# Optimization experiments

Hardware: AMD Instinct MI355X
Metric: run time of the kernel (lower is better)

Reference implementation:

```python
import jax, jax.numpy as jnp
import numpy as np

B, N, F_IN, H, FO = 4, 2048, 256, 4, 64


def setup_inputs() -> dict:
    key = jax.random.key(0)
    k1, k2, k3, k4, k5 = jax.random.split(key, 5)
    x = jax.random.normal(k1, (B, N, F_IN), dtype=jnp.float32)
    # random 0/1 adjacency with self-loops so every row of softmax is finite
    adj = jax.random.randint(k2, (N, N), 0, 2).astype(jnp.float32)
    adj = jnp.maximum(adj, jnp.eye(N, dtype=jnp.float32))
    # parameters (xavier-uniform style)
    lim_w = float(np.sqrt(6.0 / (F_IN + H * FO)))
    W = jax.random.uniform(k3, (F_IN, H * FO), minval=-lim_w, maxval=lim_w, dtype=jnp.float32)
    lim_a = float(np.sqrt(6.0 / (H + FO)))
    a_src = jax.random.uniform(k4, (H, FO), minval=-lim_a, maxval=lim_a, dtype=jnp.float32)
    a_dst = jax.random.uniform(k5, (H, FO), minval=-lim_a, maxval=lim_a, dtype=jnp.float32)
    return {"x": x, "adj": adj, "W": W, "a_src": a_src, "a_dst": a_dst}


def reference(x, adj, W, a_src, a_dst):
    # h: (B, N, H, FO)
    h = (x @ W).reshape(B, N, H, FO)
    attn_src = jnp.einsum("bnhf,hf->bnh", h, a_src)  # (B,N,H)
    attn_dst = jnp.einsum("bnhf,hf->bnh", h, a_dst)  # (B,N,H)
    # scores[b,i,j,h] = src[b,i,h] + dst[b,j,h]
    scores = attn_src[:, :, None, :] + attn_dst[:, None, :, :]
    scores = jax.nn.leaky_relu(scores, negative_slope=0.2)
    mask = (adj == 0)[None, :, :, None]  # (1,N,N,1)
    scores = jnp.where(mask, -jnp.inf, scores)
    attn = jax.nn.softmax(scores, axis=2)  # softmax over neighbors j
    # dropout is identity in eval mode / p=0
    out = jnp.einsum("bijh,bjhf->bihf", attn, h)  # (B,N,H,FO)
    return out.reshape(B, N, H * FO)  # concat=True
```

## Files before the change

### kernel.cpp

```cpp
#include <hip/hip_runtime.h>
#include <hip/hip_bf16.h>
#include <math.h>

#define B 4
#define N 2048
#define FIN 256
#define H 4
#define FO 64
#define M (B*N)
#define HF (H*FO)

typedef __attribute__((ext_vector_type(8))) short short8;
typedef __attribute__((ext_vector_type(8))) _Float16 half8;
typedef __attribute__((ext_vector_type(2))) _Float16 half2v;
typedef __attribute__((ext_vector_type(4))) float float4v;
typedef __attribute__((ext_vector_type(4))) int int4v;

#if __has_builtin(__builtin_amdgcn_exp2f)
#define EXP2(x) __builtin_amdgcn_exp2f(x)
#else
#define EXP2(x) exp2f(x)
#endif

static __device__ __forceinline__ void split_pair(float x0, float x1,
                                                  unsigned int& hi, unsigned int& lo) {
  unsigned int u0 = __builtin_bit_cast(unsigned int, x0);
  unsigned int u1 = __builtin_bit_cast(unsigned int, x1);
  hi = (u0 >> 16) | (u1 & 0xffff0000u);
  float h0 = __builtin_bit_cast(float, u0 & 0xffff0000u);
  float h1 = __builtin_bit_cast(float, u1 & 0xffff0000u);
  unsigned int l0 = __builtin_bit_cast(unsigned int, x0 - h0);
  unsigned int l1 = __builtin_bit_cast(unsigned int, x1 - h1);
  lo = (l0 >> 16) | (l1 & 0xffff0000u);
}

static __device__ __forceinline__ unsigned int fenc(float f) {
  unsigned int b = __builtin_bit_cast(unsigned int, f);
  return (b & 0x80000000u) ? ~b : (b | 0x80000000u);
}
static __device__ __forceinline__ float fdec(unsigned int e) {
  unsigned int b = (e & 0x80000000u) ? (e & 0x7fffffffu) : ~e;
  return __builtin_bit_cast(float, b);
}

static __device__ __forceinline__ unsigned int bit_sext(unsigned int v, int k) {
#if __has_builtin(__builtin_amdgcn_sbfe)
  return (unsigned int)__builtin_amdgcn_sbfe((int)v, k, 1);
#else
  return (unsigned int)(((int)(v << (31 - k))) >> 31);
#endif
}
static __device__ __forceinline__ unsigned int pm2(unsigned int mk, int p) {
  return __builtin_amdgcn_perm(bit_sext(mk, 2 * p + 1), bit_sext(mk, 2 * p), 0x07060302u);
}
static __device__ __forceinline__ unsigned int f16pk(float a, float b) {
  auto h = __builtin_amdgcn_cvt_pkrtz(a, b);
  return __builtin_bit_cast(unsigned int, h);
}

__global__ __launch_bounds__(256) void prep_wx(const float* __restrict__ Wsrc,
                                               const float* __restrict__ X,
                                               unsigned short* __restrict__ Wf_hi,
                                               unsigned short* __restrict__ Wf_lo,
                                               unsigned short* __restrict__ Xf_hi,
                                               unsigned short* __restrict__ Xf_lo,
                                               unsigned int* __restrict__ DmaxEnc) {
  const int blk = blockIdx.x;
  const int t = threadIdx.x;
  __shared__ float lds[64][65];
  if (blk < 16) {
    if (blk == 0 && t < 16) DmaxEnc[t] = 0u;
    const int k0 = (blk >> 2) * 64;
    const int h  = blk & 3;
    const int n0 = h * 64;
    const int c4 = (t & 15) * 4;
    #pragma unroll
    for (int rep = 0; rep < 4; ++rep) {
      const int kl = (t >> 4) + 16 * rep;
      const float4 v = *(const float4*)(Wsrc + (size_t)(k0 + kl) * HF + n0 + c4);
      lds[kl][c4 + 0] = v.x; lds[kl][c4 + 1] = v.y;
      lds[kl][c4 + 2] = v.z; lds[kl][c4 + 3] = v.w;
    }
    __syncthreads();
    #pragma unroll
    for (int rep = 0; rep < 2; ++rep) {
      const int s   = t + rep * 256;
      const int kcl = s >> 8;
      const int tt  = (s >> 6) & 3;
      const int ln  = s & 63;
      const int fL  = tt * 16 + (ln & 15);
      const int kb  = kcl * 32 + (ln >> 4) * 8;
      unsigned int hv[4], lv[4];
      #pragma unroll
      for (int p = 0; p < 4; ++p)
        split_pair(lds[kb + 2 * p][fL], lds[kb + 2 * p + 1][fL], hv[p], lv[p]);
      const size_t off = ((((size_t)h * 8 + (k0 >> 5) + kcl) * 4 + tt) << 9) + ln * 8;
      *(uint4*)(Wf_hi + off) = make_uint4(hv[0], hv[1], hv[2], hv[3]);
      *(uint4*)(Wf_lo + off) = make_uint4(lv[0], lv[1], lv[2], lv[3]);
    }
    return;
  }
  const int xb2   = blk - 16;
  const int xblk  = xb2 >> 2;
  const int ktile = xb2 & 3;
  const int mrow0 = xblk * 64;
  const int k0 = ktile * 64;
  const int c4 = (t & 15) * 4;
  #pragma unroll
  for (int rep = 0; rep < 4; ++rep) {
    const int rl = (t >> 4) + 16 * rep;
    const float4 v = *(const float4*)(X + (size_t)(mrow0 + rl) * FIN + k0 + c4);
    lds[rl][c4 + 0] = v.x; lds[rl][c4 + 1] = v.y;
    lds[rl][c4 + 2] = v.z; lds[rl][c4 + 3] = v.w;
  }
  __syncthreads();
  #pragma unroll
  for (int rep = 0; rep < 2; ++rep) {
    const int s   = t + rep * 256;
    const int mt  = s >> 7;
    const int kcl = (s >> 6) & 1;
    const int ln  = s & 63;
    const int mrl = mt * 16 + (ln & 15);
    const int kb  = kcl * 32 + (ln >> 4) * 8;
    unsigned int hv[4], lv[4];
    #pragma unroll
    for (int p = 0; p < 4; ++p)
      split_pair(lds[mrl][kb + 2 * p], lds[mrl][kb + 2 * p + 1], hv[p], lv[p]);
    const size_t off = (((size_t)(xblk * 4 + mt) * 8 + (ktile * 2 + kcl)) << 9) + ln * 8;
    *(uint4*)(Xf_hi + off) = make_uint4(hv[0], hv[1], hv[2], hv[3]);
    *(uint4*)(Xf_lo + off) = make_uint4(lv[0], lv[1], lv[2], lv[3]);
  }
}

__global__ __launch_bounds__(256) void gemm_fused(const unsigned short* __restrict__ Xf_hi,
                                                  const unsigned short* __restrict__ Xf_lo,
                                                  const unsigned short* __restrict__ Wf_hi,
                                                  const unsigned short* __restrict__ Wf_lo,
                                                  const float* __restrict__ adj,
                                                  const float* __restrict__ a_src,
                                                  const float* __restrict__ a_dst,
                                                  float* __restrict__ Srcv,
                                                  unsigned short* __restrict__ E1h,
                                                  unsigned short* __restrict__ E2h,
                                                  unsigned int* __restrict__ DmaxEnc,
                                                  unsigned long long* __restrict__ packed,
                                                  unsigned short* __restrict__ Hf) {
  if (blockIdx.x >= 512) {
    const int row = blockIdx.x - 512;
    const int pw = threadIdx.x >> 6, pl = threadIdx.x & 63;
    const float* ar = adj + (size_t)row * N;
    for (int c = pw; c < N / 64; c += 4) {
      unsigned long long m = __ballot(ar[c * 64 + pl] != 0.f);
      if (pl == 0) packed[(size_t)row * (N / 64) + c] = m;
    }
    return;
  }
  __shared__ unsigned short sh[64][72];
  __shared__ float smax[4];
  const int xcd  = blockIdx.x & 7;
  const int slot = blockIdx.x >> 3;
  const int mb = xcd * 16 + (slot >> 2);
  const int h  = slot & 3;
  const int w = threadIdx.x >> 6, lane = threadIdx.x & 63;
  const int fl = lane & 15, quad = lane >> 4;
  const float L2E = 1.4426950408889634f;

  const float4v zero = {0.f, 0.f, 0.f, 0.f};
  float4v acc[4] = {zero, zero, zero, zero};

  const size_t abase = (((size_t)(mb * 4 + w) * 8) << 9) + lane * 8;
  #pragma unroll
  for (int kc = 0; kc < 8; ++kc) {
    const short8 Ahi = *(const short8*)(Xf_hi + abase + ((size_t)kc << 9));
    const short8 Alo = *(const short8*)(Xf_lo + abase + ((size_t)kc << 9));
    #pragma unroll
    for (int t = 0; t < 4; ++t) {
      const size_t woff = ((((size_t)h * 8 + kc) * 4 + t) << 9) + lane * 8;
      const short8 Bhi = *(const short8*)(Wf_hi + woff);
      const short8 Blo = *(const short8*)(Wf_lo + woff);
      acc[t] = __builtin_amdgcn_mfma_f32_16x16x32_bf16(Ahi, Bhi, acc[t], 0, 0, 0);
      acc[t] = __builtin_amdgcn_mfma_f32_16x16x32_bf16(Alo, Bhi, acc[t], 0, 0, 0);
      acc[t] = __builtin_amdgcn_mfma_f32_16x16x32_bf16(Ahi, Blo, acc[t], 0, 0, 0);
    }
  }

  const int bb  = (mb * 64) >> 11;
  const int n0w = (mb * 64) & (N - 1);
  const int bh  = bb * H + h;
  float as[4], ad[4];
  #pragma unroll
  for (int t = 0; t < 4; ++t) {
    as[t] = a_src[h * FO + t * 16 + fl];
    ad[t] = a_dst[h * FO + t * 16 + fl];
  }
  float wmax = -INFINITY;
  #pragma unroll
  for (int reg = 0; reg < 4; ++reg) {
    float sv = 0.f, dv = 0.f;
    #pragma unroll
    for (int t = 0; t < 4; ++t) {
      sv = fmaf(acc[t][reg], as[t], sv);
      dv = fmaf(acc[t][reg], ad[t], dv);
    }
    #pragma unroll
    for (int off = 1; off <= 8; off <<= 1) {
      sv += __shfl_xor(sv, off, 64);
      dv += __shfl_xor(dv, off, 64);
    }
    wmax = fmaxf(wmax, dv);
    if (fl == 0) {
      const int node = n0w + w * 16 + quad * 4 + reg;
      Srcv[(bh << 11) + node] = sv;
      const unsigned int eu = f16pk(EXP2(dv * L2E),
                                    EXP2(dv * (0.2f * L2E)));
      E1h[(bh << 11) + node] = (unsigned short)(eu & 0xffffu);
      E2h[(bh << 11) + node] = (unsigned short)(eu >> 16);
    }
  }
  wmax = fmaxf(wmax, __shfl_xor(wmax, 16, 64));
  wmax = fmaxf(wmax, __shfl_xor(wmax, 32, 64));
  if (lane == 0) smax[w] = wmax;

  #pragma unroll
  for (int t = 0; t < 4; ++t) {
    const int nl = w * 16 + quad * 4;
    *(unsigned int*)&sh[t * 16 + fl][nl]     = f16pk(acc[t][0], acc[t][1]);
    *(unsigned int*)&sh[t * 16 + fl][nl + 2] = f16pk(acc[t][2], acc[t][3]);
  }
  __syncthreads();
  if (threadIdx.x == 0) {
    const float bmax = fmaxf(fmaxf(smax[0], smax[1]), fmaxf(smax[2], smax[3]));
    atomicMax(DmaxEnc + bh, fenc(bmax));
  }
  const int jc0 = n0w >> 5;
  #pragma unroll
  for (int rep = 0; rep < 2; ++rep) {
    const int s = (int)threadIdx.x + rep * 256;
    const int jcl = s >> 8;
    const int tt  = (s >> 6) & 3;
    const int ln  = s & 63;
    const int f    = tt * 16 + (ln & 15);
    const int node = jcl * 32 + (ln >> 4) * 8;
    unsigned short* dsth = Hf + (((size_t)bh * 64 + jc0 + jcl) * 4 + tt) * 512 + ln * 8;
    *(uint4*)dsth = *(const uint4*)&sh[f][node];
  }
}

__global__ __launch_bounds__(512) void gat_mfma(const unsigned char* __restrict__ pb,
                                                const float* __restrict__ Src,
                                                const unsigned short* __restrict__ E1h,
                                                const unsigned short* __restrict__ E2h,
                                                const unsigned int* __restrict__ DmaxEnc,
                                                const unsigned short* __restrict__ Hf,
                                                float* __restrict__ out) {
  const int xcd  = blockIdx.x & 7;
  const int slot = blockIdx.x >> 3;
  const int b    = xcd >> 1;
  const int i0   = ((xcd & 1) * 32 + slot) * 32;
  const int w    = threadIdx.x >> 6;
  const int lane = threadIdx.x & 63;
  const int h    = w & 3;
  const int jh   = w >> 2;
  const int bh   = b * H + h;
  const int fl   = lane & 15;
  const int kk   = (lane >> 4) * 8;
  const float L2E = 1.4426950408889634f;

  const int row0 = i0 + fl;
  const int row1 = i0 + 16 + fl;
  const float dmx = fdec(DmaxEnc[bh]);
  const float s0 = Src[(bh << 11) + row0];
  const float s1 = Src[(bh << 11) + row1];
  const float u0 = s0 + dmx, m0 = fmaxf(u0, 0.2f * u0);
  const float u1 = s1 + dmx, m1 = fmaxf(u1, 0.2f * u1);
  const float c1a = EXP2((s0 - m0) * L2E), c2a = EXP2((0.2f * s0 - m0) * L2E);
  const float c1b = EXP2((s1 - m1) * L2E), c2b = EXP2((0.2f * s1 - m1) * L2E);
  const half2v c1a2 = {(_Float16)c1a, (_Float16)c1a};
  const half2v c2a2 = {(_Float16)c2a, (_Float16)c2a};
  const half2v c1b2 = {(_Float16)c1b, (_Float16)c1b};
  const half2v c2b2 = {(_Float16)c2b, (_Float16)c2b};
  const unsigned char* pb0 = pb + (size_t)row0 * (N / 8);
  const unsigned char* pb1 = pb + (size_t)row1 * (N / 8);
  const unsigned short* hfb = Hf + (size_t)bh * 64 * 2048 + lane * 8;
  const unsigned short* e1b = E1h + (bh << 11);
  const unsigned short* e2b = E2h + (bh << 11);

  half8 ones;
  #pragma unroll
  for (int jj = 0; jj < 8; ++jj) ones[jj] = (_Float16)1.0f;

  const float4v zero = {0.f, 0.f, 0.f, 0.f};
  float4v acc[2][4];
  float4v accL[2];
  #pragma unroll
  for (int rt = 0; rt < 2; ++rt) {
    accL[rt] = zero;
    #pragma unroll
    for (int t = 0; t < 4; ++t) acc[rt][t] = zero;
  }

  const int jbeg = jh * (N / 2);
  short8 nb0, nb1, nb2, nb3;
  uint4 nE1, nE2;
  unsigned int nm0, nm1;
  {
    const unsigned short* hc = hfb + (size_t)(jbeg >> 5) * 2048;
    nb0 = *(const short8*)(hc + 0 * 512);
    nb1 = *(const short8*)(hc + 1 * 512);
    nb2 = *(const short8*)(hc + 2 * 512);
    nb3 = *(const short8*)(hc + 3 * 512);
    nE1 = *(const uint4*)(e1b + jbeg + kk);
    nE2 = *(const uint4*)(e2b + jbeg + kk);
    nm0 = pb0[(jbeg + kk) >> 3];
    nm1 = pb1[(jbeg + kk) >> 3];
  }

  for (int it = 0; it < 32; ++it) {
    const short8 b0 = nb0, b1 = nb1, b2 = nb2, b3 = nb3;
    const uint4 E1q = nE1, E2q = nE2;
    const unsigned int mk0 = nm0, mk1 = nm1;
    if (it < 31) {
      const int jn = jbeg + (it + 1) * 32;
      const unsigned short* hc = hfb + (size_t)(jn >> 5) * 2048;
      nb0 = *(const short8*)(hc + 0 * 512);
      nb1 = *(const short8*)(hc + 1 * 512);
      nb2 = *(const short8*)(hc + 2 * 512);
      nb3 = *(const short8*)(hc + 3 * 512);
      nE1 = *(const uint4*)(e1b + jn + kk);
      nE2 = *(const uint4*)(e2b + jn + kk);
      nm0 = pb0[(jn + kk) >> 3];
      nm1 = pb1[(jn + kk) >> 3];
    }
    const unsigned int e1w[4] = {E1q.x, E1q.y, E1q.z, E1q.w};
    const unsigned int e2w[4] = {E2q.x, E2q.y, E2q.z, E2q.w};
    int p0i[4], p1i[4];
    #pragma unroll
    for (int p = 0; p < 4; ++p) {
      const half2v e1 = __builtin_bit_cast(half2v, e1w[p]);
      const half2v e2 = __builtin_bit_cast(half2v, e2w[p]);
      const half2v wa = __builtin_elementwise_max(c1a2 * e1, c2a2 * e2);
      const half2v wb = __builtin_elementwise_max(c1b2 * e1, c2b2 * e2);
      p0i[p] = (int)(__builtin_bit_cast(unsigned int, wa) & pm2(mk0, p));
      p1i[p] = (int)(__builtin_bit_cast(unsigned int, wb) & pm2(mk1, p));
    }
    const half8 p0 = __builtin_bit_cast(half8, (int4v){p0i[0], p0i[1], p0i[2], p0i[3]});
    const half8 p1 = __builtin_bit_cast(half8, (int4v){p1i[0], p1i[1], p1i[2], p1i[3]});
    const half8 hb0 = __builtin_bit_cast(half8, b0);
    const half8 hb1 = __builtin_bit_cast(half8, b1);
    const half8 hb2 = __builtin_bit_cast(half8, b2);
    const half8 hb3 = __builtin_bit_cast(half8, b3);
    acc[0][0] = __builtin_amdgcn_mfma_f32_16x16x32_f16(p0, hb0, acc[0][0], 0, 0, 0);
    acc[0][1] = __builtin_amdgcn_mfma_f32_16x16x32_f16(p0, hb1, acc[0][1], 0, 0, 0);
    acc[0][2] = __builtin_amdgcn_mfma_f32_16x16x32_f16(p0, hb2, acc[0][2], 0, 0, 0);
    acc[0][3] = __builtin_amdgcn_mfma_f32_16x16x32_f16(p0, hb3, acc[0][3], 0, 0, 0);
    accL[0]   = __builtin_amdgcn_mfma_f32_16x16x32_f16(p0, ones, accL[0], 0, 0, 0);
    acc[1][0] = __builtin_amdgcn_mfma_f32_16x16x32_f16(p1, hb0, acc[1][0], 0, 0, 0);
    acc[1][1] = __builtin_amdgcn_mfma_f32_16x16x32_f16(p1, hb1, acc[1][1], 0, 0, 0);
    acc[1][2] = __builtin_amdgcn_mfma_f32_16x16x32_f16(p1, hb2, acc[1][2], 0, 0, 0);
    acc[1][3] = __builtin_amdgcn_mfma_f32_16x16x32_f16(p1, hb3, acc[1][3], 0, 0, 0);
    accL[1]   = __builtin_amdgcn_mfma_f32_16x16x32_f16(p1, ones, accL[1], 0, 0, 0);
  }

  __shared__ float4v parts[4][64][11];
  if (jh == 1) {
    #pragma unroll
    for (int rt = 0; rt < 2; ++rt) {
      #pragma unroll
      for (int t = 0; t < 4; ++t) parts[h][lane][rt * 5 + t] = acc[rt][t];
      parts[h][lane][rt * 5 + 4] = accL[rt];
    }
  }
  __syncthreads();
  if (jh == 0) {
    #pragma unroll
    for (int rt = 0; rt < 2; ++rt) {
      #pragma unroll
      for (int t = 0; t < 4; ++t) acc[rt][t] += parts[h][lane][rt * 5 + t];
      accL[rt] += parts[h][lane][rt * 5 + 4];
    }
    const int quad = lane >> 4;
    #pragma unroll
    for (int rt = 0; rt < 2; ++rt) {
      #pragma unroll
      for (int reg = 0; reg < 4; ++reg) {
        const int r = i0 + rt * 16 + quad * 4 + reg;
        const float invl = 1.f / accL[rt][reg];
        float* op = out + ((size_t)(b * N) + r) * HF + h * FO + fl;
        #pragma unroll
        for (int t = 0; t < 4; ++t) op[t * 16] = acc[rt][t][reg] * invl;
      }
    }
  }
}

extern "C" void kernel_launch(void* const* d_in, const int* in_sizes, int n_in,
                              void* d_out, int out_size, void* d_ws, size_t ws_size,
                              hipStream_t stream) {
  const float* x     = (const float*)d_in[0];
  const float* adj   = (const float*)d_in[1];
  const float* W     = (const float*)d_in[2];
  const float* a_src = (const float*)d_in[3];
  const float* a_dst = (const float*)d_in[4];
  float* out = (float*)d_out;

  char* p = (char*)d_ws;
  float* Srcv = (float*)p;                  p += (size_t)B * H * N * 4;
  unsigned short* E1h = (unsigned short*)p; p += (size_t)B * H * N * 2;
  unsigned short* E2h = (unsigned short*)p; p += (size_t)B * H * N * 2;
  unsigned int* DmaxEnc = (unsigned int*)p; p += 256;
  unsigned short* Wfh = (unsigned short*)p; p += (size_t)HF * FIN * 2;
  unsigned short* Wfl = (unsigned short*)p; p += (size_t)HF * FIN * 2;
  unsigned short* Xfh = (unsigned short*)p; p += (size_t)M * FIN * 2;
  unsigned short* Xfl = (unsigned short*)p; p += (size_t)M * FIN * 2;
  unsigned short* Hf  = (unsigned short*)p; p += (size_t)M * HF * 2;
  unsigned long long* packed = (unsigned long long*)p;

  prep_wx<<<dim3(528), dim3(256), 0, stream>>>(W, x, Wfh, Wfl, Xfh, Xfl, DmaxEnc);
  gemm_fused<<<dim3(512 + N), dim3(256), 0, stream>>>(Xfh, Xfl, Wfh, Wfl, adj,
                                                      a_src, a_dst,
                                                      Srcv, E1h, E2h, DmaxEnc,
                                                      packed, Hf);
  gat_mfma<<<dim3(B * (N / 32)), dim3(512), 0, stream>>>((const unsigned char*)packed,
                                                         Srcv, E1h, E2h, DmaxEnc, Hf, out);
}
```

Baseline: 121.9 us.

## Store adjacency as 16-bit lane masks and double-buffer chunk loads

The adjacency preprocessing now writes a full 16-bit mask per entry (0xFFFF or 0) instead of a packed bit mask. The attention kernel can then AND the fp16 weights directly with loaded mask words, dropping the per-element bit extraction and permute work. The main loop is restructured into a two-chunk ping-pong of loads and compute. The cost is 16x more mask traffic (8 MB written, and read again by every batch/head block) and extra registers for two in-flight chunks.

```diff
diff --git a/kernel.cpp b/kernel.cpp
--- a/kernel.cpp
+++ b/kernel.cpp
@@ -43,20 +43,16 @@
   return __builtin_bit_cast(float, b);
 }
 
-static __device__ __forceinline__ unsigned int bit_sext(unsigned int v, int k) {
-#if __has_builtin(__builtin_amdgcn_sbfe)
-  return (unsigned int)__builtin_amdgcn_sbfe((int)v, k, 1);
-#else
-  return (unsigned int)(((int)(v << (31 - k))) >> 31);
-#endif
-}
-static __device__ __forceinline__ unsigned int pm2(unsigned int mk, int p) {
-  return __builtin_amdgcn_perm(bit_sext(mk, 2 * p + 1), bit_sext(mk, 2 * p), 0x07060302u);
-}
 static __device__ __forceinline__ unsigned int f16pk(float a, float b) {
   auto h = __builtin_amdgcn_cvt_pkrtz(a, b);
   return __builtin_bit_cast(unsigned int, h);
 }
+
+struct Chunk {
+  short8 b0, b1, b2, b3;
+  uint4 e1, e2;
+  uint4 m0, m1;
+};
 
 __global__ __launch_bounds__(256) void prep_wx(const float* __restrict__ Wsrc,
                                                const float* __restrict__ X,
@@ -143,16 +139,19 @@
                                                   unsigned short* __restrict__ E1h,
                                                   unsigned short* __restrict__ E2h,
                                                   unsigned int* __restrict__ DmaxEnc,
-                                                  unsigned long long* __restrict__ packed,
+                                                  unsigned short* __restrict__ msk,
                                                   unsigned short* __restrict__ Hf) {
   if (blockIdx.x >= 512) {
     const int row = blockIdx.x - 512;
-    const int pw = threadIdx.x >> 6, pl = threadIdx.x & 63;
-    const float* ar = adj + (size_t)row * N;
-    for (int c = pw; c < N / 64; c += 4) {
-      unsigned long long m = __ballot(ar[c * 64 + pl] != 0.f);
-      if (pl == 0) packed[(size_t)row * (N / 64) + c] = m;
-    }
+    const int t = threadIdx.x;
+    const float* ar = adj + (size_t)row * N + t * 8;
+    const float4 v0 = *(const float4*)(ar);
+    const float4 v1 = *(const float4*)(ar + 4);
+    const unsigned int d0 = (v0.x != 0.f ? 0x0000FFFFu : 0u) | (v0.y != 0.f ? 0xFFFF0000u : 0u);
+    const unsigned int d1 = (v0.z != 0.f ? 0x0000FFFFu : 0u) | (v0.w != 0.f ? 0xFFFF0000u : 0u);
+    const unsigned int d2 = (v1.x != 0.f ? 0x0000FFFFu : 0u) | (v1.y != 0.f ? 0xFFFF0000u : 0u);
+    const unsigned int d3 = (v1.z != 0.f ? 0x0000FFFFu : 0u) | (v1.w != 0.f ? 0xFFFF0000u : 0u);
+    *(uint4*)(msk + (size_t)row * N + t * 8) = make_uint4(d0, d1, d2, d3);
     return;
   }
   __shared__ unsigned short sh[64][72];
@@ -246,7 +245,7 @@
   }
 }
 
-__global__ __launch_bounds__(512) void gat_mfma(const unsigned char* __restrict__ pb,
+__global__ __launch_bounds__(512) void gat_mfma(const unsigned short* __restrict__ msk,
                                                 const float* __restrict__ Src,
                                                 const unsigned short* __restrict__ E1h,
                                                 const unsigned short* __restrict__ E2h,
@@ -279,8 +278,8 @@
   const half2v c2a2 = {(_Float16)c2a, (_Float16)c2a};
   const half2v c1b2 = {(_Float16)c1b, (_Float16)c1b};
   const half2v c2b2 = {(_Float16)c2b, (_Float16)c2b};
-  const unsigned char* pb0 = pb + (size_t)row0 * (N / 8);
-  const unsigned char* pb1 = pb + (size_t)row1 * (N / 8);
+  const unsigned short* mr0 = msk + (size_t)row0 * N + kk;
+  const unsigned short* mr1 = msk + (size_t)row1 * N + kk;
   const unsigned short* hfb = Hf + (size_t)bh * 64 * 2048 + lane * 8;
   const unsigned short* e1b = E1h + (bh << 11);
   const unsigned short* e2b = E2h + (bh << 11);
@@ -300,39 +299,26 @@
   }
 
   const int jbeg = jh * (N / 2);
-  short8 nb0, nb1, nb2, nb3;
-  uint4 nE1, nE2;
-  unsigned int nm0, nm1;
-  {
-    const unsigned short* hc = hfb + (size_t)(jbeg >> 5) * 2048;
-    nb0 = *(const short8*)(hc + 0 * 512);
-    nb1 = *(const short8*)(hc + 1 * 512);
-    nb2 = *(const short8*)(hc + 2 * 512);
-    nb3 = *(const short8*)(hc + 3 * 512);
-    nE1 = *(const uint4*)(e1b + jbeg + kk);
-    nE2 = *(const uint4*)(e2b + jbeg + kk);
-    nm0 = pb0[(jbeg + kk) >> 3];
-    nm1 = pb1[(jbeg + kk) >> 3];
-  }
-
-  for (int it = 0; it < 32; ++it) {
-    const short8 b0 = nb0, b1 = nb1, b2 = nb2, b3 = nb3;
-    const uint4 E1q = nE1, E2q = nE2;
-    const unsigned int mk0 = nm0, mk1 = nm1;
-    if (it < 31) {
-      const int jn = jbeg + (it + 1) * 32;
-      const unsigned short* hc = hfb + (size_t)(jn >> 5) * 2048;
-      nb0 = *(const short8*)(hc + 0 * 512);
-      nb1 = *(const short8*)(hc + 1 * 512);
-      nb2 = *(const short8*)(hc + 2 * 512);
-      nb3 = *(const short8*)(hc + 3 * 512);
-      nE1 = *(const uint4*)(e1b + jn + kk);
-      nE2 = *(const uint4*)(e2b + jn + kk);
-      nm0 = pb0[(jn + kk) >> 3];
-      nm1 = pb1[(jn + kk) >> 3];
-    }
-    const unsigned int e1w[4] = {E1q.x, E1q.y, E1q.z, E1q.w};
-    const unsigned int e2w[4] = {E2q.x, E2q.y, E2q.z, E2q.w};
+
+  auto loadc = [&](int J) -> Chunk {
+    Chunk c;
+    const unsigned short* hc = hfb + (size_t)(J >> 5) * 2048;
+    c.b0 = *(const short8*)(hc + 0 * 512);
+    c.b1 = *(const short8*)(hc + 1 * 512);
+    c.b2 = *(const short8*)(hc + 2 * 512);
+    c.b3 = *(const short8*)(hc + 3 * 512);
+    c.e1 = *(const uint4*)(e1b + J + kk);
+    c.e2 = *(const uint4*)(e2b + J + kk);
+    c.m0 = *(const uint4*)(mr0 + J);
+    c.m1 = *(const uint4*)(mr1 + J);
+    return c;
+  };
+
+  auto compute = [&](const Chunk& c) {
+    const unsigned int e1w[4] = {c.e1.x, c.e1.y, c.e1.z, c.e1.w};
+    const unsigned int e2w[4] = {c.e2.x, c.e2.y, c.e2.z, c.e2.w};
+    const unsigned int m0w[4] = {c.m0.x, c.m0.y, c.m0.z, c.m0.w};
+    const unsigned int m1w[4] = {c.m1.x, c.m1.y, c.m1.z, c.m1.w};
     int p0i[4], p1i[4];
     #pragma unroll
     for (int p = 0; p < 4; ++p) {
@@ -340,15 +326,15 @@
       const half2v e2 = __builtin_bit_cast(half2v, e2w[p]);
       const half2v wa = __builtin_elementwise_max(c1a2 * e1, c2a2 * e2);
       const half2v wb = __builtin_elementwise_max(c1b2 * e1, c2b2 * e2);
-      p0i[p] = (int)(__builtin_bit_cast(unsigned int, wa) & pm2(mk0, p));
-      p1i[p] = (int)(__builtin_bit_cast(unsigned int, wb) & pm2(mk1, p));
+      p0i[p] = (int)(__builtin_bit_cast(unsigned int, wa) & m0w[p]);
+      p1i[p] = (int)(__builtin_bit_cast(unsigned int, wb) & m1w[p]);
     }
     const half8 p0 = __builtin_bit_cast(half8, (int4v){p0i[0], p0i[1], p0i[2], p0i[3]});
     const half8 p1 = __builtin_bit_cast(half8, (int4v){p1i[0], p1i[1], p1i[2], p1i[3]});
-    const half8 hb0 = __builtin_bit_cast(half8, b0);
-    const half8 hb1 = __builtin_bit_cast(half8, b1);
-    const half8 hb2 = __builtin_bit_cast(half8, b2);
-    const half8 hb3 = __builtin_bit_cast(half8, b3);
+    const half8 hb0 = __builtin_bit_cast(half8, c.b0);
+    const half8 hb1 = __builtin_bit_cast(half8, c.b1);
+    const half8 hb2 = __builtin_bit_cast(half8, c.b2);
+    const half8 hb3 = __builtin_bit_cast(half8, c.b3);
     acc[0][0] = __builtin_amdgcn_mfma_f32_16x16x32_f16(p0, hb0, acc[0][0], 0, 0, 0);
     acc[0][1] = __builtin_amdgcn_mfma_f32_16x16x32_f16(p0, hb1, acc[0][1], 0, 0, 0);
     acc[0][2] = __builtin_amdgcn_mfma_f32_16x16x32_f16(p0, hb2, acc[0][2], 0, 0, 0);
@@ -359,6 +345,19 @@
     acc[1][2] = __builtin_amdgcn_mfma_f32_16x16x32_f16(p1, hb2, acc[1][2], 0, 0, 0);
     acc[1][3] = __builtin_amdgcn_mfma_f32_16x16x32_f16(p1, hb3, acc[1][3], 0, 0, 0);
     accL[1]   = __builtin_amdgcn_mfma_f32_16x16x32_f16(p1, ones, accL[1], 0, 0, 0);
+  };
+
+  Chunk A = loadc(jbeg);
+  for (int it = 0; it < 30; it += 2) {
+    Chunk Bc = loadc(jbeg + (it + 1) * 32);
+    compute(A);
+    A = loadc(jbeg + (it + 2) * 32);
+    compute(Bc);
+  }
+  {
+    Chunk Bc = loadc(jbeg + 31 * 32);
+    compute(A);
+    compute(Bc);
   }
 
   __shared__ float4v parts[4][64][11];
@@ -413,13 +412,13 @@
   unsigned short* Xfh = (unsigned short*)p; p += (size_t)M * FIN * 2;
   unsigned short* Xfl = (unsigned short*)p; p += (size_t)M * FIN * 2;
   unsigned short* Hf  = (unsigned short*)p; p += (size_t)M * HF * 2;
-  unsigned long long* packed = (unsigned long long*)p;
+  unsigned short* msk = (unsigned short*)p;
 
   prep_wx<<<dim3(528), dim3(256), 0, stream>>>(W, x, Wfh, Wfl, Xfh, Xfl, DmaxEnc);
   gemm_fused<<<dim3(512 + N), dim3(256), 0, stream>>>(Xfh, Xfl, Wfh, Wfl, adj,
                                                       a_src, a_dst,
                                                       Srcv, E1h, E2h, DmaxEnc,
-                                                      packed, Hf);
-  gat_mfma<<<dim3(B * (N / 32)), dim3(512), 0, stream>>>((const unsigned char*)packed,
+                                                      msk, Hf);
+  gat_mfma<<<dim3(B * (N / 32)), dim3(512), 0, stream>>>(msk,
                                                          Srcv, E1h, E2h, DmaxEnc, Hf, out);
 }
```

Measured after the change: 121.6 us. No clear change (-0.2%).
